# Kernel optimization log

Measured on AMD Instinct MI355X. Metric: run time of the kernel, lower is better.

The kernel has to match this reference:

```python
import jax, jax.numpy as jnp
import numpy as np

N_HEAD = 16
NEG_INF = jnp.float32(-1e30)


def setup_inputs() -> dict:
    key = jax.random.key(0)
    k1, k2, k3 = jax.random.split(key, 3)
    B, T, C = 2, 2048, 1024
    x = jax.random.normal(k1, (B, T, C), dtype=jnp.float32)
    attn_mask = jnp.ones((B, T), dtype=jnp.int32)
    W_qkv = jax.random.normal(k2, (C, 3 * C), dtype=jnp.float32) * (1.0 / np.sqrt(C))
    b_qkv = jnp.zeros((3 * C,), dtype=jnp.float32)
    W_proj = jax.random.normal(k3, (C, C), dtype=jnp.float32) * (1.0 / np.sqrt(C))
    b_proj = jnp.zeros((C,), dtype=jnp.float32)
    return {"x": x, "attn_mask": attn_mask, "W_qkv": W_qkv, "b_qkv": b_qkv,
            "W_proj": W_proj, "b_proj": b_proj}


def reference(x, attn_mask, W_qkv, b_qkv, W_proj, b_proj):
    B, T, C = x.shape
    H = N_HEAD
    hd = C // H
    qkv = x @ W_qkv + b_qkv                       # [B,T,3C]
    q, k, v = jnp.split(qkv, 3, axis=-1)
    q = q.reshape(B, T, H, hd).transpose(0, 2, 1, 3)  # [B,H,T,hd]
    k = k.reshape(B, T, H, hd).transpose(0, 2, 1, 3)
    v = v.reshape(B, T, H, hd).transpose(0, 2, 1, 3)
    att = jnp.einsum('bhqd,bhkd->bhqk', q, k) / jnp.float32(np.sqrt(hd))  # [B,H,T,T]
    causal = jnp.tril(jnp.ones((T, T), dtype=bool))[None, None]           # [1,1,T,T]
    pad = (attn_mask != 0)[:, None, None, :]                              # [B,1,1,T]
    att = jnp.where(causal & pad, att, NEG_INF)
    att = jax.nn.softmax(att, axis=-1)
    y = jnp.einsum('bhqk,bhkd->bhqd', att, v)     # [B,H,T,hd]
    y = y.transpose(0, 2, 1, 3).reshape(B, T, C)
    return y @ W_proj + b_proj
```

## Files before the change

### kernel.cpp

```cpp
#include <hip/hip_runtime.h>

#define T_SEQ 2048
#define NHEAD 16
#define HD 64
#define CDIM 1024

typedef __bf16 bf16x8 __attribute__((ext_vector_type(8)));
typedef float f32x4 __attribute__((ext_vector_type(4)));
typedef float f32x16 __attribute__((ext_vector_type(16)));

union U16x8 { uint4 u4; unsigned short s[8]; bf16x8 b; };

__device__ __forceinline__ float bf2f(unsigned short u) {
    return __uint_as_float(((unsigned int)u) << 16);
}
__device__ __forceinline__ unsigned short f2bf(float f) {
    unsigned int u = __float_as_uint(f);
    u += 0x7fffu + ((u >> 16) & 1u);
    return (unsigned short)(u >> 16);
}
__device__ __forceinline__ U16x8 load8f(const float* __restrict__ p) {
    U16x8 r;
    float4 f0 = *(const float4*)p;
    float4 f1 = *(const float4*)(p + 4);
    r.s[0] = f2bf(f0.x); r.s[1] = f2bf(f0.y); r.s[2] = f2bf(f0.z); r.s[3] = f2bf(f0.w);
    r.s[4] = f2bf(f1.x); r.s[5] = f2bf(f1.y); r.s[6] = f2bf(f1.z); r.s[7] = f2bf(f1.w);
    return r;
}

__device__ __forceinline__ void async_copy16(const unsigned short* g, unsigned short* l) {
    __builtin_amdgcn_global_load_lds(
        (const __attribute__((address_space(1))) unsigned int*)g,
        (__attribute__((address_space(3))) unsigned int*)l, 16, 0, 0);
}

#define LOG2E 1.442695040f

#define BAR()    asm volatile("s_barrier" ::: "memory")
#define LGKM0()  asm volatile("s_waitcnt lgkmcnt(0)" ::: "memory")
#define VMC6()   asm volatile("s_waitcnt vmcnt(6)" ::: "memory")
#define VMC0()   asm volatile("s_waitcnt vmcnt(0)" ::: "memory")

__device__ __forceinline__ unsigned int cvtpk_bf16(float lo, float hi) {
    unsigned int r;
    asm("v_cvt_pk_bf16_f32 %0, %1, %2" : "=v"(r) : "v"(lo), "v"(hi));
    return r;
}
__device__ __forceinline__ void plane32swap(unsigned int &x, unsigned int &y) {
    asm("v_permlane32_swap_b32 %0, %1" : "+v"(x), "+v"(y));
}

__device__ __forceinline__ void transpose_tile(
    const float* __restrict__ in, unsigned short* __restrict__ out,
    int R, int C, int r0, int c0, float tile[64][65])
{
    const int tid = threadIdx.x;
    const int rr = tid >> 4;
    const int cc = (tid & 15) * 4;
#pragma unroll
    for (int p = 0; p < 4; ++p) {
        float4 v = *(const float4*)&in[(size_t)(r0 + p * 16 + rr) * C + c0 + cc];
        tile[p * 16 + rr][cc] = v.x;
        tile[p * 16 + rr][cc + 1] = v.y;
        tile[p * 16 + rr][cc + 2] = v.z;
        tile[p * 16 + rr][cc + 3] = v.w;
    }
    __syncthreads();
    const int n = tid >> 2;
    const int s = (tid & 3) * 8;
#pragma unroll
    for (int p = 0; p < 2; ++p) {
        const int k = s + p * 32;
        U16x8 o;
#pragma unroll
        for (int j = 0; j < 8; ++j) o.s[j] = f2bf(tile[k + j][n]);
        *(uint4*)&out[(size_t)(c0 + n) * R + r0 + k] = o.u4;
    }
}

__global__ __launch_bounds__(256) void prep(
    const float* __restrict__ X,     unsigned short* __restrict__ Xb,
    const float* __restrict__ Wqkv,  unsigned short* __restrict__ Wqkvt,
    const float* __restrict__ Wproj, unsigned short* __restrict__ Wprojt)
{
    __shared__ float tile[64][65];
    const int bid = blockIdx.x;
    if (bid < 2048) {
        const int i = (bid * 256 + threadIdx.x) * 8;
        U16x8 o = load8f(&X[i]);
        *(uint4*)&Xb[i] = o.u4;
    } else if (bid < 2816) {
        const int u = bid - 2048;
        transpose_tile(Wqkv, Wqkvt, CDIM, 3 * CDIM, (u & 15) * 64, (u >> 4) * 64, tile);
    } else {
        const int u = bid - 2816;
        transpose_tile(Wproj, Wprojt, CDIM, CDIM, (u & 15) * 64, (u >> 4) * 64, tile);
    }
}

__device__ __forceinline__ void gemm128_core(
    const unsigned short* __restrict__ A,
    const unsigned short* __restrict__ Bt,
    int K, int m0, int n0,
    unsigned short* As, unsigned short* Bs, f32x4 acc[4][4])
{
    const int tid = threadIdx.x;
    const int w = tid >> 6, lane = tid & 63;
    const int ln = lane & 15, quad = lane >> 4;
    const int wm = w >> 1, wn = w & 1;
    const int lr = lane >> 3;
    const int lc = (lane & 7) * 8;

    for (int kb = 0; kb < K; kb += 64) {
        __syncthreads();
#pragma unroll
        for (int i = 0; i < 4; ++i) {
            async_copy16(&A[(size_t)(m0 + w * 32 + i * 8 + lr) * K + kb + lc],
                         &As[(w * 32 + i * 8) * 64]);
            async_copy16(&Bt[(size_t)(n0 + w * 32 + i * 8 + lr) * K + kb + lc],
                         &Bs[(w * 32 + i * 8) * 64]);
        }
        __syncthreads();
#pragma unroll
        for (int kk = 0; kk < 2; ++kk) {
            U16x8 af[4], bff[4];
#pragma unroll
            for (int i = 0; i < 4; ++i)
                af[i].u4 = *(const uint4*)&As[(wm * 64 + i * 16 + ln) * 64 + kk * 32 + quad * 8];
#pragma unroll
            for (int j = 0; j < 4; ++j)
                bff[j].u4 = *(const uint4*)&Bs[(wn * 64 + j * 16 + ln) * 64 + kk * 32 + quad * 8];
#pragma unroll
            for (int i = 0; i < 4; ++i)
#pragma unroll
                for (int j = 0; j < 4; ++j)
                    acc[i][j] = __builtin_amdgcn_mfma_f32_16x16x32_bf16(af[i].b, bff[j].b, acc[i][j], 0, 0, 0);
        }
    }
}

__device__ __forceinline__ void stageA(const unsigned short* __restrict__ A,
                                       unsigned short* buf,
                                       int m0, int t, int unit, int w, int lane)
{
#pragma unroll
    for (int s = 0; s < 2; ++s) {
        const int r0 = s * 128 + unit * 64 + w * 8;
        const int row = r0 + (lane >> 3);
        const int col = (16 * (lane & 7)) ^ ((row & 4) ? 32 : 0);
        const unsigned short* src = A + (size_t)(m0 + row) * CDIM + t * 64 + (col >> 1);
        async_copy16(src, buf + r0 * 64);
    }
}

__device__ __forceinline__ void stageB(const unsigned short* __restrict__ B,
                                       unsigned short* buf,
                                       int n0, int t, int unit, int w, int lane)
{
#pragma unroll
    for (int s = 0; s < 2; ++s) {
        const int slice = s * 8 + w;
        const int r0 = (slice >> 2) * 64 + unit * 32 + (slice & 3) * 8;
        const int row = r0 + (lane >> 3);
        const int col = (16 * (lane & 7)) ^ ((row & 4) ? 32 : 0);
        const unsigned short* src = B + (size_t)(n0 + row) * CDIM + t * 64 + (col >> 1);
        async_copy16(src, buf + r0 * 64);
    }
}

__device__ __forceinline__ void readA(U16x8 af[4][2], const unsigned short* buf,
                                      int wm, int qm, int ln, int quad)
{
#pragma unroll
    for (int i = 0; i < 4; ++i) {
        const int row = wm * 128 + qm * 64 + i * 16 + ln;
        const int sw = (row & 4) ? 32 : 0;
#pragma unroll
        for (int kk = 0; kk < 2; ++kk) {
            const int byt = row * 128 + ((kk * 64 + quad * 16) ^ sw);
            af[i][kk].u4 = *(const uint4*)((const char*)buf + byt);
        }
    }
}

__device__ __forceinline__ void readB(U16x8 bf[2][2], const unsigned short* buf,
                                      int wn, int qn, int ln, int quad)
{
#pragma unroll
    for (int jj = 0; jj < 2; ++jj) {
        const int row = wn * 64 + qn * 32 + jj * 16 + ln;
        const int sw = (row & 4) ? 32 : 0;
#pragma unroll
        for (int kk = 0; kk < 2; ++kk) {
            const int byt = row * 128 + ((kk * 64 + quad * 16) ^ sw);
            bf[jj][kk].u4 = *(const uint4*)((const char*)buf + byt);
        }
    }
}

template<int QM, int QN>
__device__ __forceinline__ void mfma16(f32x4 acc[8][4], const U16x8 af[4][2],
                                       const U16x8 bf[2][2])
{
    __builtin_amdgcn_s_setprio(1);
#pragma unroll
    for (int i = 0; i < 4; ++i)
#pragma unroll
        for (int jj = 0; jj < 2; ++jj)
#pragma unroll
            for (int kk = 0; kk < 2; ++kk)
                acc[QM * 4 + i][QN * 2 + jj] = __builtin_amdgcn_mfma_f32_16x16x32_bf16(
                    af[i][kk].b, bf[jj][kk].b, acc[QM * 4 + i][QN * 2 + jj], 0, 0, 0);
    __builtin_amdgcn_s_setprio(0);
}

__global__ __launch_bounds__(512) void qkv8(
    const unsigned short* __restrict__ Xb,
    const unsigned short* __restrict__ Wt,
    const float* __restrict__ bias,
    unsigned short* __restrict__ Qp,
    unsigned short* __restrict__ Kp,
    unsigned short* __restrict__ Vtp)
{
    __shared__ __align__(1024) unsigned short smem[4][16384];
    unsigned short* Ab0 = smem[0];
    unsigned short* Ab1 = smem[1];
    unsigned short* Bb0 = smem[2];
    unsigned short* Bb1 = smem[3];

    const int tid = threadIdx.x;
    const int w = tid >> 6, lane = tid & 63;
    const int ln = lane & 15, quad = lane >> 4;
    const int wm = w >> 2, wn = w & 3;

    const int bid = blockIdx.x;
    const int swz = (bid & 7) * 24 + (bid >> 3);
    const int nt = swz % 12, mt = swz / 12;
    const int m0 = mt * 256, n0 = nt * 256;

    f32x4 acc[8][4];
#pragma unroll
    for (int i = 0; i < 8; ++i)
#pragma unroll
        for (int j = 0; j < 4; ++j) acc[i][j] = (f32x4){0.f, 0.f, 0.f, 0.f};

    stageA(Xb, Ab0, m0, 0, 0, w, lane);
    stageB(Wt, Bb0, n0, 0, 0, w, lane);
    stageB(Wt, Bb0, n0, 0, 1, w, lane);
    stageA(Xb, Ab0, m0, 0, 1, w, lane);
    stageA(Xb, Ab1, m0, 1, 0, w, lane);
    stageB(Wt, Bb1, n0, 1, 0, w, lane);
    stageB(Wt, Bb1, n0, 1, 1, w, lane);
    VMC6();
    BAR();

    U16x8 af[4][2], bq0[2][2], bq1[2][2];

    for (int j = 0; j < 7; ++j) {
        const int e = 2 * j, o = 2 * j + 1;
        readA(af, Ab0, wm, 0, ln, quad);
        readB(bq0, Bb0, wn, 0, ln, quad);
        stageA(Xb, Ab1, m0, o, 1, w, lane);
        BAR(); LGKM0();
        mfma16<0, 0>(acc, af, bq0);
        LGKM0(); BAR();
        readB(bq1, Bb0, wn, 1, ln, quad);
        stageA(Xb, Ab0, m0, e + 2, 0, w, lane);
        BAR(); LGKM0();
        mfma16<0, 1>(acc, af, bq1);
        LGKM0(); BAR();
        readA(af, Ab0, wm, 1, ln, quad);
        stageB(Wt, Bb0, n0, e + 2, 0, w, lane);
        BAR(); LGKM0();
        mfma16<1, 0>(acc, af, bq0);
        LGKM0(); BAR();
        stageB(Wt, Bb0, n0, e + 2, 1, w, lane);
        BAR();
        mfma16<1, 1>(acc, af, bq1);
        VMC6(); BAR();
        readA(af, Ab1, wm, 0, ln, quad);
        readB(bq0, Bb1, wn, 0, ln, quad);
        stageA(Xb, Ab0, m0, e + 2, 1, w, lane);
        BAR(); LGKM0();
        mfma16<0, 0>(acc, af, bq0);
        LGKM0(); BAR();
        readB(bq1, Bb1, wn, 1, ln, quad);
        stageA(Xb, Ab1, m0, o + 2, 0, w, lane);
        BAR(); LGKM0();
        mfma16<0, 1>(acc, af, bq1);
        LGKM0(); BAR();
        readA(af, Ab1, wm, 1, ln, quad);
        stageB(Wt, Bb1, n0, o + 2, 0, w, lane);
        BAR(); LGKM0();
        mfma16<1, 0>(acc, af, bq0);
        LGKM0(); BAR();
        stageB(Wt, Bb1, n0, o + 2, 1, w, lane);
        BAR();
        mfma16<1, 1>(acc, af, bq1);
        VMC6(); BAR();
    }

    stageA(Xb, Ab1, m0, 15, 1, w, lane);
    VMC0(); BAR();

    readA(af, Ab0, wm, 0, ln, quad);
    readB(bq0, Bb0, wn, 0, ln, quad);
    readB(bq1, Bb0, wn, 1, ln, quad);
    mfma16<0, 0>(acc, af, bq0);
    mfma16<0, 1>(acc, af, bq1);
    readA(af, Ab0, wm, 1, ln, quad);
    mfma16<1, 0>(acc, af, bq0);
    mfma16<1, 1>(acc, af, bq1);

    readA(af, Ab1, wm, 0, ln, quad);
    readB(bq0, Bb1, wn, 0, ln, quad);
    readB(bq1, Bb1, wn, 1, ln, quad);
    mfma16<0, 0>(acc, af, bq0);
    mfma16<0, 1>(acc, af, bq1);
    readA(af, Ab1, wm, 1, ln, quad);
    mfma16<1, 0>(acc, af, bq0);
    mfma16<1, 1>(acc, af, bq1);

    const int which = n0 >> 10;
    float bv[4];
#pragma unroll
    for (int jj = 0; jj < 4; ++jj) bv[jj] = bias[n0 + wn * 64 + jj * 16 + ln];

    if (which < 2) {
        unsigned short* dst = (which == 0) ? Qp : Kp;
        const float qsc = (which == 0) ? 0.125f : 1.0f;
#pragma unroll
        for (int jj = 0; jj < 4; ++jj) {
            const int n = n0 + wn * 64 + jj * 16 + ln;
            const int h = (n >> 6) & 15, d = n & 63;
#pragma unroll
            for (int i = 0; i < 8; ++i)
#pragma unroll
                for (int r = 0; r < 4; ++r) {
                    const int m = m0 + wm * 128 + i * 16 + quad * 4 + r;
                    const int b = m >> 11, tt = m & 2047;
                    dst[(((size_t)(b * NHEAD + h) * T_SEQ) + tt) * HD + d] =
                        f2bf((acc[i][jj][r] + bv[jj]) * qsc);
                }
        }
    } else {
#pragma unroll
        for (int jj = 0; jj < 4; ++jj) {
            const int n = n0 + wn * 64 + jj * 16 + ln;
            const int c = n - 2048;
#pragma unroll
            for (int i = 0; i < 8; ++i) {
                const int m00 = m0 + wm * 128 + i * 16 + quad * 4;
                const int b = m00 >> 11, tt = m00 & 2047;
                ushort4 pk;
                pk.x = f2bf(acc[i][jj][0] + bv[jj]);
                pk.y = f2bf(acc[i][jj][1] + bv[jj]);
                pk.z = f2bf(acc[i][jj][2] + bv[jj]);
                pk.w = f2bf(acc[i][jj][3] + bv[jj]);
                *(ushort4*)&Vtp[(size_t)(b * 1024 + c) * T_SEQ + tt] = pk;
            }
        }
    }
}

__global__ __launch_bounds__(256) void proj_gemm(
    const unsigned short* __restrict__ Yin,
    const unsigned short* __restrict__ Wt,
    const float* __restrict__ bias,
    float* __restrict__ out)
{
    __shared__ unsigned short As[128 * 64];
    __shared__ unsigned short Bs[128 * 64];
    const int m0 = blockIdx.y * 128;
    const int n0 = blockIdx.x * 128;

    f32x4 acc[4][4];
#pragma unroll
    for (int i = 0; i < 4; ++i)
#pragma unroll
        for (int j = 0; j < 4; ++j) acc[i][j] = (f32x4){0.f, 0.f, 0.f, 0.f};

    gemm128_core(Yin, Wt, CDIM, m0, n0, As, Bs, acc);

    const int tid = threadIdx.x;
    const int w = tid >> 6, lane = tid & 63;
    const int ln = lane & 15, quad = lane >> 4;
    const int wm = w >> 1, wn = w & 1;

#pragma unroll
    for (int j = 0; j < 4; ++j) {
        const int n = n0 + wn * 64 + j * 16 + ln;
        const float bv = bias[n];
#pragma unroll
        for (int i = 0; i < 4; ++i)
#pragma unroll
            for (int r = 0; r < 4; ++r) {
                const int m = m0 + wm * 64 + i * 16 + quad * 4 + r;
                out[(size_t)m * CDIM + n] = acc[i][j][r] + bv;
            }
    }
}


__device__ __forceinline__ int swz(int row, int slot) {
    return row * 64 + ((slot ^ (row & 7)) << 3);
}

__global__ __launch_bounds__(256) void flash_attn32(
    const unsigned short* __restrict__ Qp,
    const unsigned short* __restrict__ Kp,
    const unsigned short* __restrict__ Vtp,
    const int* __restrict__ mask,
    unsigned short* __restrict__ Y,
    unsigned short* __restrict__ Po,
    float* __restrict__ Pm,
    float* __restrict__ Pl)
{
    __shared__ unsigned short Ks[64 * 64];
    __shared__ unsigned short Vs[64 * 64];
    __shared__ float mask_arr[64];
    __shared__ float als[4][32];
    __shared__ int flagu;

    const int bh = blockIdx.x;
    const int y = blockIdx.y;
    int qb, j0, jstep;
    bool split;
    if (y < 32)      { qb = 15 - (y >> 2);        j0 = y & 3;        jstep = 4; split = true; }
    else if (y < 40) { qb = 7 - ((y - 32) >> 1);  j0 = (y - 32) & 1; jstep = 2; split = true; }
    else             { qb = 43 - y;               j0 = 0;            jstep = 1; split = false; }
    const int pidx = split
        ? ((qb < 8) ? (bh * 40 + (qb - 4) * 2 + j0)
                    : (bh * 40 + 8 + (qb - 8) * 4 + j0))
        : 0;

    const int b = bh >> 4, h = bh & 15;
    const int tid = threadIdx.x;
    const int w = tid >> 6, lane = tid & 63;
    const int l31 = lane & 31, hi = lane >> 5;
    const int row8 = tid >> 3, seg = tid & 7;
    const size_t base = (size_t)bh * T_SEQ * HD;
    const int qB = qb * 128;
    const int qw0 = qB + w * 32;
    const int qv = qw0 + l31;
    const int jlast = 2 * qb + 1;

    U16x8 qf[4];
    {
        const unsigned short* qrow = &Qp[base + (size_t)qv * HD];
#pragma unroll
        for (int c = 0; c < 4; ++c)
            qf[c].u4 = *(const uint4*)&qrow[c * 16 + hi * 8];
    }

    f32x16 oA0, oA1;
#pragma unroll
    for (int r = 0; r < 16; ++r) { oA0[r] = 0.f; oA1[r] = 0.f; }
    float m_r = -3.0e38f, mL = 0.f, l_r = 0.f;

    uint4 kr0, kr1, vr0, vr1;
    float mf = 0.f;
    {
        const unsigned short* kp0 = &Kp[base + (size_t)(j0 * 64 + row8) * HD + seg * 8];
        kr0 = *(const uint4*)kp0;
        kr1 = *(const uint4*)(kp0 + 32 * HD);
        const unsigned short* vp0 = &Vtp[base + (size_t)row8 * T_SEQ + j0 * 64 + seg * 8];
        vr0 = *(const uint4*)vp0;
        vr1 = *(const uint4*)(vp0 + 32 * T_SEQ);
        if (tid < 64) mf = mask[b * T_SEQ + j0 * 64 + tid] ? 0.f : -1.0e30f;
    }

    for (int j = j0; j <= jlast; j += jstep) {
        __syncthreads();
        *(uint4*)&Ks[swz(row8, seg)]      = kr0;
        *(uint4*)&Ks[swz(row8 + 32, seg)] = kr1;
        *(uint4*)&Vs[swz(row8, seg)]      = vr0;
        *(uint4*)&Vs[swz(row8 + 32, seg)] = vr1;
        if (w == 0) {
            const int k = lane;
            const int idx = ((k >> 2) & 1) * 32 + (k >> 5) * 16 + ((k & 31) >> 3) * 4 + (k & 3);
            mask_arr[idx] = mf;
            const unsigned long long bb = __ballot(mf == 0.f);
            if (lane == 0) flagu = (bb == 0xFFFFFFFFFFFFFFFFull) ? 0 : 1;
        }
        __syncthreads();

        const int jn = j + jstep;
        if (jn <= jlast) {
            const unsigned short* kp0 = &Kp[base + (size_t)(jn * 64 + row8) * HD + seg * 8];
            kr0 = *(const uint4*)kp0;
            kr1 = *(const uint4*)(kp0 + 32 * HD);
            const unsigned short* vp0 = &Vtp[base + (size_t)row8 * T_SEQ + jn * 64 + seg * 8];
            vr0 = *(const uint4*)vp0;
            vr1 = *(const uint4*)(vp0 + 32 * T_SEQ);
            if (tid < 64) mf = mask[b * T_SEQ + jn * 64 + tid] ? 0.f : -1.0e30f;
        }

        const bool skipw = (j * 64 > qw0 + 31);
        if (!skipw) {
            const bool edge = (j * 64 + 63 > qw0);
            const int anymask = flagu;

            f32x16 sc0, sc1;
#pragma unroll
            for (int r = 0; r < 16; ++r) { sc0[r] = 0.f; sc1[r] = 0.f; }
#pragma unroll
            for (int c = 0; c < 4; ++c) {
                U16x8 ka0, ka1;
                const int r0 = l31, r1 = 32 + l31;
                ka0.u4 = *(const uint4*)&Ks[r0 * 64 + (((2 * c + hi) ^ (r0 & 7)) << 3)];
                ka1.u4 = *(const uint4*)&Ks[r1 * 64 + (((2 * c + hi) ^ (r1 & 7)) << 3)];
                sc0 = __builtin_amdgcn_mfma_f32_32x32x16_bf16(ka0.b, qf[c].b, sc0, 0, 0, 0);
                sc1 = __builtin_amdgcn_mfma_f32_32x32x16_bf16(ka1.b, qf[c].b, sc1, 0, 0, 0);
            }

            if (anymask) {
#pragma unroll
                for (int g = 0; g < 4; ++g) {
                    const f32x4 m0v = *(const f32x4*)&mask_arr[hi * 32 + g * 4];
                    const f32x4 m1v = *(const f32x4*)&mask_arr[hi * 32 + 16 + g * 4];
#pragma unroll
                    for (int t = 0; t < 4; ++t) {
                        sc0[g * 4 + t] += m0v[t];
                        sc1[g * 4 + t] += m1v[t];
                    }
                }
            }
            if (edge) {
#pragma unroll
                for (int r = 0; r < 16; ++r) {
                    const int krow = (r & 3) + 8 * (r >> 2) + 4 * hi;
                    if (j * 64 + krow > qv)      sc0[r] = -1.0e30f;
                    if (j * 64 + 32 + krow > qv) sc1[r] = -1.0e30f;
                }
            }

            float tm = -3.0e38f;
#pragma unroll
            for (int r = 0; r < 16; ++r)
                tm = fmaxf(tm, fmaxf(sc0[r], sc1[r]));
            tm = fmaxf(tm, __shfl_xor(tm, 32));

            if (__any(tm > m_r + 8.f)) {
                const float mn = fmaxf(m_r, tm);
                const float a = __builtin_amdgcn_exp2f((m_r - mn) * LOG2E);
                m_r = mn; mL = mn * LOG2E;
                l_r *= a;
                if (hi == 0) als[w][l31] = a;
                f32x4 av[4];
#pragma unroll
                for (int g = 0; g < 4; ++g)
                    av[g] = *(const f32x4*)&als[w][g * 8 + hi * 4];
#pragma unroll
                for (int r = 0; r < 16; ++r) {
                    const float aa = av[r >> 2][r & 3];
                    oA0[r] *= aa; oA1[r] *= aa;
                }
            }

            float ps = 0.f;
#pragma unroll
            for (int r = 0; r < 16; ++r) {
                const float p0 = __builtin_amdgcn_exp2f(fmaf(sc0[r], LOG2E, -mL));
                const float p1 = __builtin_amdgcn_exp2f(fmaf(sc1[r], LOG2E, -mL));
                sc0[r] = p0; sc1[r] = p1;
                ps += p0 + p1;
            }
            l_r += ps;

#pragma unroll
            for (int c = 0; c < 4; ++c) {
                const int rb = (c & 1) * 8;
                unsigned int x0, y0, x1, y1;
                if (c < 2) {
                    x0 = cvtpk_bf16(sc0[rb + 0], sc0[rb + 1]);
                    y0 = cvtpk_bf16(sc0[rb + 4], sc0[rb + 5]);
                    x1 = cvtpk_bf16(sc0[rb + 2], sc0[rb + 3]);
                    y1 = cvtpk_bf16(sc0[rb + 6], sc0[rb + 7]);
                } else {
                    x0 = cvtpk_bf16(sc1[rb + 0], sc1[rb + 1]);
                    y0 = cvtpk_bf16(sc1[rb + 4], sc1[rb + 5]);
                    x1 = cvtpk_bf16(sc1[rb + 2], sc1[rb + 3]);
                    y1 = cvtpk_bf16(sc1[rb + 6], sc1[rb + 7]);
                }
                plane32swap(x0, y0);
                plane32swap(x1, y1);
                U16x8 pa;
                pa.u4 = make_uint4(x0, x1, y0, y1);
                {
                    const int vr_0 = l31, vr_1 = 32 + l31;
                    U16x8 vb0, vb1;
                    vb0.u4 = *(const uint4*)&Vs[vr_0 * 64 + (((2 * c + hi) ^ (vr_0 & 7)) << 3)];
                    vb1.u4 = *(const uint4*)&Vs[vr_1 * 64 + (((2 * c + hi) ^ (vr_1 & 7)) << 3)];
                    oA0 = __builtin_amdgcn_mfma_f32_32x32x16_bf16(pa.b, vb0.b, oA0, 0, 0, 0);
                    oA1 = __builtin_amdgcn_mfma_f32_32x32x16_bf16(pa.b, vb1.b, oA1, 0, 0, 0);
                }
            }
        }
    }

    const float lt = l_r + __shfl_xor(l_r, 32);

    if (split) {
        if (hi == 0) {
            Pm[pidx * 128 + w * 32 + l31] = m_r;
            Pl[pidx * 128 + w * 32 + l31] = lt;
        }
#pragma unroll
        for (int r = 0; r < 16; ++r) {
            const int qlc = w * 32 + (r & 3) + 8 * (r >> 2) + 4 * hi;
            Po[(size_t)pidx * 8192 + qlc * 64 + l31]      = f2bf(oA0[r]);
            Po[(size_t)pidx * 8192 + qlc * 64 + 32 + l31] = f2bf(oA1[r]);
        }
    } else {
        if (hi == 0) als[w][l31] = 1.0f / lt;
        f32x4 lv[4];
#pragma unroll
        for (int g = 0; g < 4; ++g)
            lv[g] = *(const f32x4*)&als[w][g * 8 + hi * 4];
#pragma unroll
        for (int r = 0; r < 16; ++r) {
            const int q = qw0 + (r & 3) + 8 * (r >> 2) + 4 * hi;
            const float sl = lv[r >> 2][r & 3];
            const size_t row = (size_t)(b * T_SEQ + q);
            Y[row * CDIM + h * HD + l31]      = f2bf(oA0[r] * sl);
            Y[row * CDIM + h * HD + 32 + l31] = f2bf(oA1[r] * sl);
        }
    }
}

__global__ __launch_bounds__(256) void merge_attn(
    const unsigned short* __restrict__ Po,
    const float* __restrict__ Pm, const float* __restrict__ Pl,
    unsigned short* __restrict__ Y)
{
    const int u = blockIdx.x;
    const int bh = u & 31;
    const int v = u >> 5;
    const int qb = 4 + (v >> 2), part = v & 3;
    const int tid = threadIdx.x;
    const int ql = part * 32 + (tid >> 3);
    const int d0 = (tid & 7) * 8;
    const int b = bh >> 4, h = bh & 15;

    int S, basei;
    if (qb < 8) { S = 2; basei = bh * 40 + (qb - 4) * 2; }
    else        { S = 4; basei = bh * 40 + 8 + (qb - 8) * 4; }

    float mv[4], lv[4];
    float M = -3.0e38f;
#pragma unroll
    for (int s = 0; s < 4; ++s) {
        if (s < S) {
            mv[s] = Pm[(basei + s) * 128 + ql];
            lv[s] = Pl[(basei + s) * 128 + ql];
            M = fmaxf(M, mv[s]);
        }
    }
    float f[4], L = 0.f;
#pragma unroll
    for (int s = 0; s < 4; ++s) {
        if (s < S) {
            f[s] = __builtin_amdgcn_exp2f((mv[s] - M) * LOG2E);
            L += f[s] * lv[s];
        }
    }
    const float inv = 1.0f / L;

    float o[8] = {0.f, 0.f, 0.f, 0.f, 0.f, 0.f, 0.f, 0.f};
#pragma unroll
    for (int s = 0; s < 4; ++s) {
        if (s < S) {
            U16x8 a;
            a.u4 = *(const uint4*)&Po[(size_t)(basei + s) * 8192 + ql * 64 + d0];
#pragma unroll
            for (int j = 0; j < 8; ++j) o[j] += f[s] * bf2f(a.s[j]);
        }
    }

    U16x8 ot;
#pragma unroll
    for (int j = 0; j < 8; ++j) ot.s[j] = f2bf(o[j] * inv);

    const int q = qb * 128 + ql;
    *(uint4*)&Y[(size_t)(b * T_SEQ + q) * CDIM + h * HD + d0] = ot.u4;
}

extern "C" void kernel_launch(void* const* d_in, const int* in_sizes, int n_in,
                              void* d_out, int out_size, void* d_ws, size_t ws_size,
                              hipStream_t stream)
{
    const float* X     = (const float*)d_in[0];
    const int*   mask  = (const int*)d_in[1];
    const float* Wqkv  = (const float*)d_in[2];
    const float* bqkv  = (const float*)d_in[3];
    const float* Wproj = (const float*)d_in[4];
    const float* bproj = (const float*)d_in[5];
    float* out = (float*)d_out;

    const size_t per = (size_t)2 * NHEAD * T_SEQ * HD;
    unsigned short* Qp     = (unsigned short*)d_ws;
    unsigned short* Kp     = Qp + per;
    unsigned short* Vtp    = Kp + per;
    unsigned short* Xb     = Vtp + per;
    unsigned short* Yp     = Xb;
    unsigned short* Wprojt = Xb + per;
    unsigned short* Wqkvt  = Wprojt + (size_t)CDIM * CDIM;
    unsigned short* Po     = Wqkvt;
    float*          Pm     = (float*)(Po + (size_t)1280 * 8192);
    float*          Pl     = Pm + 1280 * 128;

    prep<<<3072, 256, 0, stream>>>(X, Xb, Wqkv, Wqkvt, Wproj, Wprojt);
    qkv8<<<192, 512, 0, stream>>>(Xb, Wqkvt, bqkv, Qp, Kp, Vtp);
    flash_attn32<<<dim3(2 * NHEAD, 44), 256, 0, stream>>>(Qp, Kp, Vtp, mask, Yp, Po, Pm, Pl);
    merge_attn<<<1536, 256, 0, stream>>>(Po, Pm, Pl, Yp);
    proj_gemm<<<dim3(8, 32), 256, 0, stream>>>(Yp, Wprojt, bproj, out);
}
```

Before: 209.5 us.

## Double-buffer K/V tiles in attention using async global-to-LDS copies

Replaces the register-staged K/V prefetch with direct async global-to-LDS copies into a two-slot shared memory buffer, so the next tile loads while the current one is computed. The swizzle moves into the global source address so that LDS writes land in the same XOR layout. The two barriers per iteration become one wait-plus-barrier at the end of each iteration. This doubles LDS use for K/V and the mask, which may lower occupancy, and it relies on async_copy16/VMC0 helpers defined elsewhere in the file.

```diff
diff --git a/kernel.cpp b/kernel.cpp
--- a/kernel.cpp
+++ b/kernel.cpp
@@ -402,10 +402,6 @@
 }
 
 
-__device__ __forceinline__ int swz(int row, int slot) {
-    return row * 64 + ((slot ^ (row & 7)) << 3);
-}
-
 __global__ __launch_bounds__(256) void flash_attn32(
     const unsigned short* __restrict__ Qp,
     const unsigned short* __restrict__ Kp,
@@ -416,11 +412,11 @@
     float* __restrict__ Pm,
     float* __restrict__ Pl)
 {
-    __shared__ unsigned short Ks[64 * 64];
-    __shared__ unsigned short Vs[64 * 64];
-    __shared__ float mask_arr[64];
+    __shared__ unsigned short Ks[2][64 * 64];
+    __shared__ unsigned short Vs[2][64 * 64];
+    __shared__ float mask_arr[2][64];
     __shared__ float als[4][32];
-    __shared__ int flagu;
+    __shared__ int flagu[2];
 
     const int bh = blockIdx.x;
     const int y = blockIdx.y;
@@ -438,13 +434,16 @@
     const int tid = threadIdx.x;
     const int w = tid >> 6, lane = tid & 63;
     const int l31 = lane & 31, hi = lane >> 5;
-    const int row8 = tid >> 3, seg = tid & 7;
     const size_t base = (size_t)bh * T_SEQ * HD;
     const int qB = qb * 128;
     const int qw0 = qB + w * 32;
     const int qv = qw0 + l31;
     const int jlast = 2 * qb + 1;
 
+    const int rw0 = w * 8;
+    const int rl = lane >> 3;
+    const int sc8 = (((lane & 7) ^ rl) & 7) * 8;
+
     U16x8 qf[4];
     {
         const unsigned short* qrow = &Qp[base + (size_t)qv * HD];
@@ -458,48 +457,48 @@
     for (int r = 0; r < 16; ++r) { oA0[r] = 0.f; oA1[r] = 0.f; }
     float m_r = -3.0e38f, mL = 0.f, l_r = 0.f;
 
-    uint4 kr0, kr1, vr0, vr1;
-    float mf = 0.f;
     {
-        const unsigned short* kp0 = &Kp[base + (size_t)(j0 * 64 + row8) * HD + seg * 8];
-        kr0 = *(const uint4*)kp0;
-        kr1 = *(const uint4*)(kp0 + 32 * HD);
-        const unsigned short* vp0 = &Vtp[base + (size_t)row8 * T_SEQ + j0 * 64 + seg * 8];
-        vr0 = *(const uint4*)vp0;
-        vr1 = *(const uint4*)(vp0 + 32 * T_SEQ);
-        if (tid < 64) mf = mask[b * T_SEQ + j0 * 64 + tid] ? 0.f : -1.0e30f;
-    }
-
-    for (int j = j0; j <= jlast; j += jstep) {
-        __syncthreads();
-        *(uint4*)&Ks[swz(row8, seg)]      = kr0;
-        *(uint4*)&Ks[swz(row8 + 32, seg)] = kr1;
-        *(uint4*)&Vs[swz(row8, seg)]      = vr0;
-        *(uint4*)&Vs[swz(row8 + 32, seg)] = vr1;
+        const int t = j0;
+        async_copy16(&Kp[base + (size_t)(t * 64 + rw0 + rl) * HD + sc8],      &Ks[0][rw0 * 64]);
+        async_copy16(&Kp[base + (size_t)(t * 64 + 32 + rw0 + rl) * HD + sc8], &Ks[0][(rw0 + 32) * 64]);
+        async_copy16(&Vtp[base + (size_t)(rw0 + rl) * T_SEQ + t * 64 + sc8],      &Vs[0][rw0 * 64]);
+        async_copy16(&Vtp[base + (size_t)(32 + rw0 + rl) * T_SEQ + t * 64 + sc8], &Vs[0][(rw0 + 32) * 64]);
         if (w == 0) {
+            const float mfv = mask[b * T_SEQ + t * 64 + lane] ? 0.f : -1.0e30f;
             const int k = lane;
             const int idx = ((k >> 2) & 1) * 32 + (k >> 5) * 16 + ((k & 31) >> 3) * 4 + (k & 3);
-            mask_arr[idx] = mf;
-            const unsigned long long bb = __ballot(mf == 0.f);
-            if (lane == 0) flagu = (bb == 0xFFFFFFFFFFFFFFFFull) ? 0 : 1;
-        }
-        __syncthreads();
-
+            mask_arr[0][idx] = mfv;
+            const unsigned long long bb = __ballot(mfv == 0.f);
+            if (lane == 0) flagu[0] = (bb == 0xFFFFFFFFFFFFFFFFull) ? 0 : 1;
+        }
+    }
+    VMC0(); LGKM0(); BAR();
+
+    int p = 0;
+    for (int j = j0; j <= jlast; j += jstep) {
         const int jn = j + jstep;
         if (jn <= jlast) {
-            const unsigned short* kp0 = &Kp[base + (size_t)(jn * 64 + row8) * HD + seg * 8];
-            kr0 = *(const uint4*)kp0;
-            kr1 = *(const uint4*)(kp0 + 32 * HD);
-            const unsigned short* vp0 = &Vtp[base + (size_t)row8 * T_SEQ + jn * 64 + seg * 8];
-            vr0 = *(const uint4*)vp0;
-            vr1 = *(const uint4*)(vp0 + 32 * T_SEQ);
-            if (tid < 64) mf = mask[b * T_SEQ + jn * 64 + tid] ? 0.f : -1.0e30f;
+            const int t = jn, q = p ^ 1;
+            async_copy16(&Kp[base + (size_t)(t * 64 + rw0 + rl) * HD + sc8],      &Ks[q][rw0 * 64]);
+            async_copy16(&Kp[base + (size_t)(t * 64 + 32 + rw0 + rl) * HD + sc8], &Ks[q][(rw0 + 32) * 64]);
+            async_copy16(&Vtp[base + (size_t)(rw0 + rl) * T_SEQ + t * 64 + sc8],      &Vs[q][rw0 * 64]);
+            async_copy16(&Vtp[base + (size_t)(32 + rw0 + rl) * T_SEQ + t * 64 + sc8], &Vs[q][(rw0 + 32) * 64]);
+            if (w == 0) {
+                const float mfv = mask[b * T_SEQ + t * 64 + lane] ? 0.f : -1.0e30f;
+                const int k = lane;
+                const int idx = ((k >> 2) & 1) * 32 + (k >> 5) * 16 + ((k & 31) >> 3) * 4 + (k & 3);
+                mask_arr[q][idx] = mfv;
+                const unsigned long long bb = __ballot(mfv == 0.f);
+                if (lane == 0) flagu[q] = (bb == 0xFFFFFFFFFFFFFFFFull) ? 0 : 1;
+            }
         }
 
         const bool skipw = (j * 64 > qw0 + 31);
         if (!skipw) {
             const bool edge = (j * 64 + 63 > qw0);
-            const int anymask = flagu;
+            const int anymask = flagu[p];
+            const unsigned short* KsP = Ks[p];
+            const unsigned short* VsP = Vs[p];
 
             f32x16 sc0, sc1;
 #pragma unroll
@@ -508,8 +507,8 @@
             for (int c = 0; c < 4; ++c) {
                 U16x8 ka0, ka1;
                 const int r0 = l31, r1 = 32 + l31;
-                ka0.u4 = *(const uint4*)&Ks[r0 * 64 + (((2 * c + hi) ^ (r0 & 7)) << 3)];
-                ka1.u4 = *(const uint4*)&Ks[r1 * 64 + (((2 * c + hi) ^ (r1 & 7)) << 3)];
+                ka0.u4 = *(const uint4*)&KsP[r0 * 64 + (((2 * c + hi) ^ (r0 & 7)) << 3)];
+                ka1.u4 = *(const uint4*)&KsP[r1 * 64 + (((2 * c + hi) ^ (r1 & 7)) << 3)];
                 sc0 = __builtin_amdgcn_mfma_f32_32x32x16_bf16(ka0.b, qf[c].b, sc0, 0, 0, 0);
                 sc1 = __builtin_amdgcn_mfma_f32_32x32x16_bf16(ka1.b, qf[c].b, sc1, 0, 0, 0);
             }
@@ -517,8 +516,8 @@
             if (anymask) {
 #pragma unroll
                 for (int g = 0; g < 4; ++g) {
-                    const f32x4 m0v = *(const f32x4*)&mask_arr[hi * 32 + g * 4];
-                    const f32x4 m1v = *(const f32x4*)&mask_arr[hi * 32 + 16 + g * 4];
+                    const f32x4 m0v = *(const f32x4*)&mask_arr[p][hi * 32 + g * 4];
+                    const f32x4 m1v = *(const f32x4*)&mask_arr[p][hi * 32 + 16 + g * 4];
 #pragma unroll
                     for (int t = 0; t < 4; ++t) {
                         sc0[g * 4 + t] += m0v[t];
@@ -590,13 +589,16 @@
                 {
                     const int vr_0 = l31, vr_1 = 32 + l31;
                     U16x8 vb0, vb1;
-                    vb0.u4 = *(const uint4*)&Vs[vr_0 * 64 + (((2 * c + hi) ^ (vr_0 & 7)) << 3)];
-                    vb1.u4 = *(const uint4*)&Vs[vr_1 * 64 + (((2 * c + hi) ^ (vr_1 & 7)) << 3)];
+                    vb0.u4 = *(const uint4*)&VsP[vr_0 * 64 + (((2 * c + hi) ^ (vr_0 & 7)) << 3)];
+                    vb1.u4 = *(const uint4*)&VsP[vr_1 * 64 + (((2 * c + hi) ^ (vr_1 & 7)) << 3)];
                     oA0 = __builtin_amdgcn_mfma_f32_32x32x16_bf16(pa.b, vb0.b, oA0, 0, 0, 0);
                     oA1 = __builtin_amdgcn_mfma_f32_32x32x16_bf16(pa.b, vb1.b, oA1, 0, 0, 0);
                 }
             }
         }
+
+        VMC0(); LGKM0(); BAR();
+        p ^= 1;
     }
 
     const float lt = l_r + __shfl_xor(l_r, 32);
```

After: 206.7 us. Within noise of the previous version (-1.3%).
